# Performance work log

Measured on AMD Instinct MI355X. Metric: run time of the kernel, lower is better.

## Reference

```python
import jax, jax.numpy as jnp
import numpy as np

N_NODES = 50000
N_EDGES = 800000
D = 128


def setup_inputs() -> dict:
    key = jax.random.key(0)
    ks = jax.random.split(key, 8)
    h = jax.random.normal(ks[0], (N_NODES, D), dtype=jnp.float32)
    src = jax.random.randint(ks[1], (N_EDGES,), 0, N_NODES, dtype=jnp.int64)
    dst = jax.random.randint(ks[2], (N_EDGES,), 0, N_NODES, dtype=jnp.int64)
    # Glorot-ish init for the three GraphConv weights
    scale = 1.0 / np.sqrt(D)
    W0 = jax.random.normal(ks[3], (D, D), dtype=jnp.float32) * scale
    W1 = jax.random.normal(ks[4], (D, D), dtype=jnp.float32) * scale
    W2 = jax.random.normal(ks[5], (D, D), dtype=jnp.float32) * scale
    b0 = jnp.zeros((D,), dtype=jnp.float32)
    b1 = jnp.zeros((D,), dtype=jnp.float32)
    b2 = jnp.zeros((D,), dtype=jnp.float32)
    return {"h": h, "src": src, "dst": dst, "W0": W0, "b0": b0,
            "W1": W1, "b1": b1, "W2": W2, "b2": b2}


def _graph_conv(x, src, dst, W, b, n_nodes):
    """DGL GraphConv, norm='both', activation=ReLU.
    in_feats == out_feats -> aggregate first, then matmul W."""
    ones = jnp.ones_like(src, dtype=x.dtype)
    out_deg = jnp.clip(jax.ops.segment_sum(ones, src, num_segments=n_nodes), 1.0)
    in_deg = jnp.clip(jax.ops.segment_sum(ones, dst, num_segments=n_nodes), 1.0)
    x = x * (out_deg ** -0.5)[:, None]          # src-side normalization
    m = jax.ops.segment_sum(x[src], dst, num_segments=n_nodes)  # sparse aggregation
    m = m * (in_deg ** -0.5)[:, None]           # dst-side normalization
    return jax.nn.relu(m @ W + b)


def reference(h, src, dst, W0, b0, W1, b1, W2, b2):
    n = h.shape[0]
    h = _graph_conv(h, src, dst, W0, b0, n)
    h = _graph_conv(h, src, dst, W1, b1, n)
    h = _graph_conv(h, src, dst, W2, b2, n)
    return h
```

## Files before the change

kernel.cpp:

```cpp
#include <hip/hip_runtime.h>

#define N_NODES 50000
#define N_EDGES 800000
#define D 128
#define CAP 48
#define MS_STRIDE 132
#define QNODES 12500
#define QWORDS (QNODES / 4)
#define HISTB 1024
#define EPB (N_EDGES / 256)
#define HWORDS (N_NODES / 4)
#define FILLB ((N_EDGES + 255) / 256)
#define REDB ((HWORDS + 255) / 256)

typedef __attribute__((ext_vector_type(4))) float f32x4;
typedef __attribute__((ext_vector_type(8))) short s16x8;

__device__ inline unsigned short f32_to_bf16_rtne(float f) {
    union { float f; unsigned u; } c; c.f = f;
    unsigned u = c.u;
    u += 0x7FFF + ((u >> 16) & 1);
    return (unsigned short)(u >> 16);
}
__device__ inline float bf16_to_f32(unsigned short h) {
    union { unsigned u; float f; } c; c.u = ((unsigned)h) << 16;
    return c.f;
}
__device__ inline unsigned pack_bf2(float a, float b) {
    return (unsigned)f32_to_bf16_rtne(a) | ((unsigned)f32_to_bf16_rtne(b) << 16);
}
__device__ inline void unpack_bf2(unsigned u, float& a, float& b) {
    union { unsigned u; float f; } c0, c1;
    c0.u = u << 16; c1.u = u & 0xFFFF0000u;
    a = c0.f; b = c1.f;
}
__device__ inline void acc_uint4(uint4 v, float* a) {
    float f0, f1;
    unpack_bf2(v.x, f0, f1); a[0] += f0; a[1] += f1;
    unpack_bf2(v.y, f0, f1); a[2] += f0; a[3] += f1;
    unpack_bf2(v.z, f0, f1); a[4] += f0; a[5] += f1;
    unpack_bf2(v.w, f0, f1); a[6] += f0; a[7] += f1;
}


__global__ __launch_bounds__(256) void build_all(const int* __restrict__ src,
                                                 const int* __restrict__ dst,
                                                 int* __restrict__ cursor,
                                                 unsigned* __restrict__ partial,
                                                 int* __restrict__ slots) {
    __shared__ unsigned hist[QWORDS];
    int b = blockIdx.x;
    if (b < HISTB) {
        int q = b >> 8, p = b & 255;
        int n0 = q * QNODES;
        for (int i = threadIdx.x; i < QWORDS; i += 256) hist[i] = 0;
        __syncthreads();
        int e0 = p * EPB;
        for (int i = threadIdx.x; i < EPB; i += 256) {
            int s = src[e0 + i];
            unsigned r = (unsigned)(s - n0);
            if (r < (unsigned)QNODES) atomicAdd(&hist[r >> 2], 1u << ((r & 3) * 8));
        }
        __syncthreads();
        unsigned* dstp = partial + (size_t)b * QWORDS;
        for (int i = threadIdx.x; i < QWORDS; i += 256) dstp[i] = hist[i];
    } else {
        int e = (b - HISTB) * 256 + threadIdx.x;
        if (e < N_EDGES) {
            int d = dst[e], s = src[e];
            int pos = atomicAdd(&cursor[d], 1);
            if (pos < CAP) slots[d * CAP + pos] = s;
        }
    }
}


__global__ __launch_bounds__(256) void mid_reduce_pack(const unsigned* __restrict__ partial,
                                                       float* __restrict__ s_out,
                                                       const float* __restrict__ W0,
                                                       const float* __restrict__ W1,
                                                       const float* __restrict__ W2,
                                                       s16x8* __restrict__ wpk) {
    int blk = blockIdx.x;
    if (blk < REDB) {
        int w = blk * 256 + threadIdx.x;
        if (w >= HWORDS) return;
        int q = w / QWORDS, wq = w - q * QWORDS;
        const unsigned* base = partial + (size_t)(q * 256) * QWORDS + wq;
        int c0 = 0, c1 = 0, c2 = 0, c3 = 0;
        for (int p = 0; p < 256; p++) {
            unsigned v = base[(size_t)p * QWORDS];
            c0 += v & 255; c1 += (v >> 8) & 255; c2 += (v >> 16) & 255; c3 += v >> 24;
        }
        float4 so;
        so.x = rsqrtf(fmaxf((float)c0, 1.0f));
        so.y = rsqrtf(fmaxf((float)c1, 1.0f));
        so.z = rsqrtf(fmaxf((float)c2, 1.0f));
        so.w = rsqrtf(fmaxf((float)c3, 1.0f));
        ((float4*)s_out)[w] = so;
    } else {
        int wid = (blk - REDB) * 4 + (threadIdx.x >> 6);
        if (wid >= 96) return;
        int lane = threadIdx.x & 63;
        int layer = wid / 32, rem = wid % 32;
        int ct = rem >> 2, ks = rem & 3;
        const float* W = (layer == 0) ? W0 : (layer == 1) ? W1 : W2;
        int col = ct * 16 + (lane & 15);
        int k0  = ks * 32 + (lane >> 4) * 8;
        s16x8 hi, lo;
#pragma unroll
        for (int j = 0; j < 8; j++) {
            float w = W[(k0 + j) * D + col];
            unsigned short h = f32_to_bf16_rtne(w);
            hi[j] = (short)h;
            lo[j] = (short)f32_to_bf16_rtne(w - bf16_to_f32(h));
        }
        int idx = layer * 4096 + (ct * 4 + ks) * 64 + lane;
        wpk[idx]        = hi;
        wpk[idx + 2048] = lo;
    }
}


__global__ __launch_bounds__(256) void hconv(const float4* __restrict__ h,
                                             const float* __restrict__ s_out,
                                             uint2* __restrict__ hbA,
                                             uint2* __restrict__ hbB) {
    int gid = blockIdx.x * 256 + threadIdx.x;
    const int total = N_NODES * 32;
    if (gid < total) {
        float so = s_out[gid >> 5];
        float4 v = h[gid];
        hbA[gid] = make_uint2(pack_bf2(so * v.x, so * v.y), pack_bf2(so * v.z, so * v.w));
    } else if (gid < total + 32) {
        hbA[total + (gid - total)] = make_uint2(0u, 0u);
    } else if (gid < total + 64) {
        hbB[total + (gid - total - 32)] = make_uint2(0u, 0u);
    }
}


__global__ __launch_bounds__(256) void fused_layer(const uint4* __restrict__ x,
                                                   const int* __restrict__ slots,
                                                   const int* __restrict__ deg,
                                                   const s16x8* __restrict__ wpk,
                                                   const float* __restrict__ bias,
                                                   const float* __restrict__ s_out,
                                                   float* __restrict__ outf,
                                                   unsigned short* __restrict__ outb) {
    __shared__ float mS[16 * MS_STRIDE];
    int tid = threadIdx.x;
    int row0 = blockIdx.x * 16;

    {
        int nloc = tid >> 4;
        int l    = tid & 15;
        int node = row0 + nloc;
        int dgraw = deg[node];
        int dg = min(dgraw, CAP);
        int base = node * CAP;
        int idx0 = (l      < dg) ? slots[base + l]      : N_NODES;
        int idx1 = (16 + l < dg) ? slots[base + 16 + l] : N_NODES;
        int idx2 = (32 + l < dg) ? slots[base + 32 + l] : N_NODES;

        float a[8];
#pragma unroll
        for (int j = 0; j < 8; j++) a[j] = 0.f;

        int nr = (dg + 7) >> 3;
        for (int r = 0; r < nr; r++) {
            int c = r >> 1;
            int v = (c == 0) ? idx0 : ((c == 1) ? idx1 : idx2);
            int k = (r & 1) * 8;
            int s0 = __shfl(v, k + 0, 16), s1 = __shfl(v, k + 1, 16);
            int s2 = __shfl(v, k + 2, 16), s3 = __shfl(v, k + 3, 16);
            int s4 = __shfl(v, k + 4, 16), s5 = __shfl(v, k + 5, 16);
            int s6 = __shfl(v, k + 6, 16), s7 = __shfl(v, k + 7, 16);
            uint4 g0 = x[s0 * 16 + l];
            uint4 g1 = x[s1 * 16 + l];
            uint4 g2 = x[s2 * 16 + l];
            uint4 g3 = x[s3 * 16 + l];
            uint4 g4 = x[s4 * 16 + l];
            uint4 g5 = x[s5 * 16 + l];
            uint4 g6 = x[s6 * 16 + l];
            uint4 g7 = x[s7 * 16 + l];
            acc_uint4(g0, a); acc_uint4(g1, a); acc_uint4(g2, a); acc_uint4(g3, a);
            acc_uint4(g4, a); acc_uint4(g5, a); acc_uint4(g6, a); acc_uint4(g7, a);
        }
        float si = rsqrtf(fmaxf((float)dgraw, 1.0f));
        float* dp = &mS[nloc * MS_STRIDE + l * 8];
#pragma unroll
        for (int j = 0; j < 8; j++) dp[j] = a[j] * si;
    }
    __syncthreads();

    int wv = tid >> 6;
    int lane = tid & 63;
    int arow = lane & 15, aq = lane >> 4;
    int ct0 = wv * 2, ct1 = ct0 + 1;
    f32x4 acc0 = (f32x4)0.f, acc1 = (f32x4)0.f;

#pragma unroll
    for (int ks = 0; ks < 4; ks++) {
        const float* ap = &mS[arow * MS_STRIDE + ks * 32 + aq * 8];
        s16x8 ahi, alo;
#pragma unroll
        for (int j = 0; j < 8; j++) {
            float av = ap[j];
            unsigned short hh = f32_to_bf16_rtne(av);
            ahi[j] = (short)hh;
            alo[j] = (short)f32_to_bf16_rtne(av - bf16_to_f32(hh));
        }
        int idx0 = (ct0 * 4 + ks) * 64 + lane;
        int idx1 = (ct1 * 4 + ks) * 64 + lane;
        s16x8 b0h = wpk[idx0], b0l = wpk[idx0 + 2048];
        s16x8 b1h = wpk[idx1], b1l = wpk[idx1 + 2048];
        acc0 = __builtin_amdgcn_mfma_f32_16x16x32_bf16(ahi, b0h, acc0, 0, 0, 0);
        acc0 = __builtin_amdgcn_mfma_f32_16x16x32_bf16(alo, b0h, acc0, 0, 0, 0);
        acc0 = __builtin_amdgcn_mfma_f32_16x16x32_bf16(ahi, b0l, acc0, 0, 0, 0);
        acc1 = __builtin_amdgcn_mfma_f32_16x16x32_bf16(ahi, b1h, acc1, 0, 0, 0);
        acc1 = __builtin_amdgcn_mfma_f32_16x16x32_bf16(alo, b1h, acc1, 0, 0, 0);
        acc1 = __builtin_amdgcn_mfma_f32_16x16x32_bf16(ahi, b1l, acc1, 0, 0, 0);
    }

    int crow0 = aq * 4;
    float so4[4];
    if (outb) {
#pragma unroll
        for (int r = 0; r < 4; r++) so4[r] = s_out[row0 + crow0 + r];
    }
    int colA = ct0 * 16 + arow, colB = ct1 * 16 + arow;
    float bA = bias[colA], bB = bias[colB];
#pragma unroll
    for (int r = 0; r < 4; r++) {
        size_t rowoff = (size_t)(row0 + crow0 + r) * D;
        float vA = fmaxf(acc0[r] + bA, 0.f);
        float vB = fmaxf(acc1[r] + bB, 0.f);
        if (outf) { outf[rowoff + colA] = vA; outf[rowoff + colB] = vB; }
        if (outb) {
            outb[rowoff + colA] = f32_to_bf16_rtne(so4[r] * vA);
            outb[rowoff + colB] = f32_to_bf16_rtne(so4[r] * vB);
        }
    }
}


extern "C" void kernel_launch(void* const* d_in, const int* in_sizes, int n_in,
                              void* d_out, int out_size, void* d_ws, size_t ws_size,
                              hipStream_t stream) {
    const float* h  = (const float*)d_in[0];
    const int*  src = (const int*)d_in[1];
    const int*  dst = (const int*)d_in[2];
    const float* W0 = (const float*)d_in[3];
    const float* b0 = (const float*)d_in[4];
    const float* W1 = (const float*)d_in[5];
    const float* b1 = (const float*)d_in[6];
    const float* W2 = (const float*)d_in[7];
    const float* b2 = (const float*)d_in[8];
    float* out = (float*)d_out;

    char* w = (char*)d_ws;
    auto carve = [&](size_t bytes) -> void* {
        void* p = (void*)w;
        w += (bytes + 255) & ~(size_t)255;
        return p;
    };
    int*      cursor  = (int*)carve(N_NODES * sizeof(int));
    float*    s_out   = (float*)carve(N_NODES * sizeof(float));
    int*      slots   = (int*)carve((size_t)N_NODES * CAP * sizeof(int));
    unsigned* partial = (unsigned*)carve((size_t)HISTB * QWORDS * sizeof(unsigned));
    unsigned short* actA = (unsigned short*)carve((size_t)(N_NODES + 1) * D * 2);
    unsigned short* actB = (unsigned short*)carve((size_t)(N_NODES + 1) * D * 2);
    s16x8*    wpk     = (s16x8*)carve(3 * 4096 * sizeof(s16x8));

    hipMemsetAsync(cursor, 0, N_NODES * sizeof(int), stream);
    build_all<<<HISTB + FILLB, 256, 0, stream>>>(src, dst, cursor, partial, slots);
    mid_reduce_pack<<<REDB + 24, 256, 0, stream>>>(partial, s_out, W0, W1, W2, wpk);
    hconv<<<(N_NODES * 32 + 64 + 255) / 256, 256, 0, stream>>>((const float4*)h, s_out,
                                                               (uint2*)actA, (uint2*)actB);

    const int GRID = N_NODES / 16;

    fused_layer<<<GRID, 256, 0, stream>>>((const uint4*)actA, slots, cursor,
                                          wpk, b0, s_out, nullptr, actB);
    fused_layer<<<GRID, 256, 0, stream>>>((const uint4*)actB, slots, cursor,
                                          wpk + 4096, b1, s_out, nullptr, actA);
    fused_layer<<<GRID, 256, 0, stream>>>((const uint4*)actA, slots, cursor,
                                          wpk + 8192, b2, s_out, out, nullptr);
}
```

Baseline: 261.0 us.

## Split bf16 activations into four column-quarter planes and gather per quarter

Stores the bf16 activation tables as four separate planes, each holding a 32-column quarter for every node (64 bytes per node per plane). The aggregation loop now makes four passes, one per quarter. In each pass, 4 lanes cover a row slice and 4 edge groups run in parallel, and the partial sums are reduced with cross-lane shuffles. The aim is to shrink the gather working set per pass so it fits in cache better. The change also adds nontemporal loads and stores for slots and outputs. In exchange the slot indices are walked four times and shuffle/reduction work is added.

```diff
diff --git a/kernel.cpp b/kernel.cpp
--- a/kernel.cpp
+++ b/kernel.cpp
@@ -12,9 +12,11 @@
 #define HWORDS (N_NODES / 4)
 #define FILLB ((N_EDGES + 255) / 256)
 #define REDB ((HWORDS + 255) / 256)
+#define NP1 (N_NODES + 1)
 
 typedef __attribute__((ext_vector_type(4))) float f32x4;
 typedef __attribute__((ext_vector_type(8))) short s16x8;
+typedef __attribute__((ext_vector_type(4))) unsigned u32x4;
 
 __device__ inline unsigned short f32_to_bf16_rtne(float f) {
     union { float f; unsigned u; } c; c.f = f;
@@ -34,7 +36,7 @@
     c0.u = u << 16; c1.u = u & 0xFFFF0000u;
     a = c0.f; b = c1.f;
 }
-__device__ inline void acc_uint4(uint4 v, float* a) {
+__device__ inline void acc_u32x4(u32x4 v, float* a) {
     float f0, f1;
     unpack_bf2(v.x, f0, f1); a[0] += f0; a[1] += f1;
     unpack_bf2(v.y, f0, f1); a[2] += f0; a[3] += f1;
@@ -124,23 +126,33 @@
 
 __global__ __launch_bounds__(256) void hconv(const float4* __restrict__ h,
                                              const float* __restrict__ s_out,
-                                             uint2* __restrict__ hbA,
-                                             uint2* __restrict__ hbB) {
+                                             u32x4* __restrict__ actA,
+                                             u32x4* __restrict__ actB) {
     int gid = blockIdx.x * 256 + threadIdx.x;
-    const int total = N_NODES * 32;
+    const int total = N_NODES * 16;
     if (gid < total) {
-        float so = s_out[gid >> 5];
-        float4 v = h[gid];
-        hbA[gid] = make_uint2(pack_bf2(so * v.x, so * v.y), pack_bf2(so * v.z, so * v.w));
+        int q = gid / (N_NODES * 4);
+        int r = gid - q * (N_NODES * 4);
+        int node = r >> 2, p = r & 3;
+        int part = q * 4 + p;
+        float so = s_out[node];
+        float4 v0 = h[node * 32 + part * 2];
+        float4 v1 = h[node * 32 + part * 2 + 1];
+        u32x4 u;
+        u.x = pack_bf2(so * v0.x, so * v0.y); u.y = pack_bf2(so * v0.z, so * v0.w);
+        u.z = pack_bf2(so * v1.x, so * v1.y); u.w = pack_bf2(so * v1.z, so * v1.w);
+        __builtin_nontemporal_store(u, &actA[(size_t)(q * NP1 + node) * 4 + p]);
+    } else if (gid < total + 16) {
+        int z = gid - total;
+        actA[(size_t)((z >> 2) * NP1 + N_NODES) * 4 + (z & 3)] = (u32x4)0u;
     } else if (gid < total + 32) {
-        hbA[total + (gid - total)] = make_uint2(0u, 0u);
-    } else if (gid < total + 64) {
-        hbB[total + (gid - total - 32)] = make_uint2(0u, 0u);
-    }
-}
-
-
-__global__ __launch_bounds__(256) void fused_layer(const uint4* __restrict__ x,
+        int z = gid - total - 16;
+        actB[(size_t)((z >> 2) * NP1 + N_NODES) * 4 + (z & 3)] = (u32x4)0u;
+    }
+}
+
+
+__global__ __launch_bounds__(256) void fused_layer(const u32x4* __restrict__ x,
                                                    const int* __restrict__ slots,
                                                    const int* __restrict__ deg,
                                                    const s16x8* __restrict__ wpk,
@@ -155,42 +167,46 @@
     {
         int nloc = tid >> 4;
         int l    = tid & 15;
+        int eh   = l >> 2, p = l & 3;
         int node = row0 + nloc;
         int dgraw = deg[node];
         int dg = min(dgraw, CAP);
         int base = node * CAP;
-        int idx0 = (l      < dg) ? slots[base + l]      : N_NODES;
-        int idx1 = (16 + l < dg) ? slots[base + 16 + l] : N_NODES;
-        int idx2 = (32 + l < dg) ? slots[base + 32 + l] : N_NODES;
-
-        float a[8];
-#pragma unroll
-        for (int j = 0; j < 8; j++) a[j] = 0.f;
-
-        int nr = (dg + 7) >> 3;
-        for (int r = 0; r < nr; r++) {
-            int c = r >> 1;
-            int v = (c == 0) ? idx0 : ((c == 1) ? idx1 : idx2);
-            int k = (r & 1) * 8;
-            int s0 = __shfl(v, k + 0, 16), s1 = __shfl(v, k + 1, 16);
-            int s2 = __shfl(v, k + 2, 16), s3 = __shfl(v, k + 3, 16);
-            int s4 = __shfl(v, k + 4, 16), s5 = __shfl(v, k + 5, 16);
-            int s6 = __shfl(v, k + 6, 16), s7 = __shfl(v, k + 7, 16);
-            uint4 g0 = x[s0 * 16 + l];
-            uint4 g1 = x[s1 * 16 + l];
-            uint4 g2 = x[s2 * 16 + l];
-            uint4 g3 = x[s3 * 16 + l];
-            uint4 g4 = x[s4 * 16 + l];
-            uint4 g5 = x[s5 * 16 + l];
-            uint4 g6 = x[s6 * 16 + l];
-            uint4 g7 = x[s7 * 16 + l];
-            acc_uint4(g0, a); acc_uint4(g1, a); acc_uint4(g2, a); acc_uint4(g3, a);
-            acc_uint4(g4, a); acc_uint4(g5, a); acc_uint4(g6, a); acc_uint4(g7, a);
-        }
+        int idx0 = (l      < dg) ? __builtin_nontemporal_load(&slots[base + l])      : N_NODES;
+        int idx1 = (16 + l < dg) ? __builtin_nontemporal_load(&slots[base + 16 + l]) : N_NODES;
+        int idx2 = (32 + l < dg) ? __builtin_nontemporal_load(&slots[base + 32 + l]) : N_NODES;
         float si = rsqrtf(fmaxf((float)dgraw, 1.0f));
-        float* dp = &mS[nloc * MS_STRIDE + l * 8];
-#pragma unroll
-        for (int j = 0; j < 8; j++) dp[j] = a[j] * si;
+        int nit = (dg + 7) >> 3;
+
+        for (int q = 0; q < 4; q++) {
+            const u32x4* xq = x + (size_t)(q * NP1) * 4;
+            float a[8];
+#pragma unroll
+            for (int j = 0; j < 8; j++) a[j] = 0.f;
+            for (int it = 0; it < nit; it++) {
+                int e0 = it * 8 + eh, e1 = it * 8 + 4 + eh;
+                int c0 = e0 >> 4, k0 = e0 & 15;
+                int c1 = e1 >> 4, k1 = e1 & 15;
+                int v0 = (c0 == 0) ? idx0 : ((c0 == 1) ? idx1 : idx2);
+                int v1 = (c1 == 0) ? idx0 : ((c1 == 1) ? idx1 : idx2);
+                int s0 = __shfl(v0, k0, 16);
+                int s1 = __shfl(v1, k1, 16);
+                u32x4 g0 = xq[s0 * 4 + p];
+                u32x4 g1 = xq[s1 * 4 + p];
+                acc_u32x4(g0, a);
+                acc_u32x4(g1, a);
+            }
+#pragma unroll
+            for (int j = 0; j < 8; j++) {
+                a[j] += __shfl_xor(a[j], 4, 16);
+                a[j] += __shfl_xor(a[j], 8, 16);
+            }
+            if (eh == 0) {
+                float* dp = &mS[nloc * MS_STRIDE + q * 32 + p * 8];
+#pragma unroll
+                for (int j = 0; j < 8; j++) dp[j] = a[j] * si;
+            }
+        }
     }
     __syncthreads();
 
@@ -230,16 +246,21 @@
         for (int r = 0; r < 4; r++) so4[r] = s_out[row0 + crow0 + r];
     }
     int colA = ct0 * 16 + arow, colB = ct1 * 16 + arow;
+    int wcA = colA & 31, wcB = colB & 31;
     float bA = bias[colA], bB = bias[colB];
 #pragma unroll
     for (int r = 0; r < 4; r++) {
-        size_t rowoff = (size_t)(row0 + crow0 + r) * D;
+        int row = row0 + crow0 + r;
         float vA = fmaxf(acc0[r] + bA, 0.f);
         float vB = fmaxf(acc1[r] + bB, 0.f);
-        if (outf) { outf[rowoff + colA] = vA; outf[rowoff + colB] = vB; }
+        if (outf) {
+            __builtin_nontemporal_store(vA, &outf[(size_t)row * D + colA]);
+            __builtin_nontemporal_store(vB, &outf[(size_t)row * D + colB]);
+        }
         if (outb) {
-            outb[rowoff + colA] = f32_to_bf16_rtne(so4[r] * vA);
-            outb[rowoff + colB] = f32_to_bf16_rtne(so4[r] * vB);
+            size_t qb = (size_t)(wv * NP1 + row) * 32;
+            __builtin_nontemporal_store(f32_to_bf16_rtne(so4[r] * vA), &outb[qb + wcA]);
+            __builtin_nontemporal_store(f32_to_bf16_rtne(so4[r] * vB), &outb[qb + wcB]);
         }
     }
 }
@@ -269,22 +290,22 @@
     float*    s_out   = (float*)carve(N_NODES * sizeof(float));
     int*      slots   = (int*)carve((size_t)N_NODES * CAP * sizeof(int));
     unsigned* partial = (unsigned*)carve((size_t)HISTB * QWORDS * sizeof(unsigned));
-    unsigned short* actA = (unsigned short*)carve((size_t)(N_NODES + 1) * D * 2);
-    unsigned short* actB = (unsigned short*)carve((size_t)(N_NODES + 1) * D * 2);
+    unsigned short* actA = (unsigned short*)carve((size_t)NP1 * 256);
+    unsigned short* actB = (unsigned short*)carve((size_t)NP1 * 256);
     s16x8*    wpk     = (s16x8*)carve(3 * 4096 * sizeof(s16x8));
 
-    hipMemsetAsync(cursor, 0, N_NODES * sizeof(int), stream);
+    (void)hipMemsetAsync(cursor, 0, N_NODES * sizeof(int), stream);
     build_all<<<HISTB + FILLB, 256, 0, stream>>>(src, dst, cursor, partial, slots);
     mid_reduce_pack<<<REDB + 24, 256, 0, stream>>>(partial, s_out, W0, W1, W2, wpk);
-    hconv<<<(N_NODES * 32 + 64 + 255) / 256, 256, 0, stream>>>((const float4*)h, s_out,
-                                                               (uint2*)actA, (uint2*)actB);
+    hconv<<<(N_NODES * 16 + 32 + 255) / 256, 256, 0, stream>>>((const float4*)h, s_out,
+                                                               (u32x4*)actA, (u32x4*)actB);
 
     const int GRID = N_NODES / 16;
 
-    fused_layer<<<GRID, 256, 0, stream>>>((const uint4*)actA, slots, cursor,
+    fused_layer<<<GRID, 256, 0, stream>>>((const u32x4*)actA, slots, cursor,
                                           wpk, b0, s_out, nullptr, actB);
-    fused_layer<<<GRID, 256, 0, stream>>>((const uint4*)actB, slots, cursor,
+    fused_layer<<<GRID, 256, 0, stream>>>((const u32x4*)actB, slots, cursor,
                                           wpk + 4096, b1, s_out, nullptr, actA);
-    fused_layer<<<GRID, 256, 0, stream>>>((const uint4*)actA, slots, cursor,
+    fused_layer<<<GRID, 256, 0, stream>>>((const u32x4*)actA, slots, cursor,
                                           wpk + 8192, b2, s_out, out, nullptr);
 }
```

New measurement: 293.7 us. +12.5%, slower.

## Bucket nodes by in-degree iteration count to balance fused layer blocks

Applied to the files above, without the earlier changes.

Adds two small kernels that count nodes per gather-iteration bucket (ceil(min(deg,CAP)/8)) and scatter node ids into a permutation grouped by bucket. Each fused_layer block then processes 16 nodes of similar degree, read through the permutation, and writes outputs to the permuted rows. The aim is to cut divergence within 16-lane groups and wavefronts, where the slowest node's degree sets the loop count. The cost is two extra launches, indirect row addressing and scattered output writes.

```diff
diff --git a/kernel.cpp b/kernel.cpp
--- a/kernel.cpp
+++ b/kernel.cpp
@@ -12,6 +12,7 @@
 #define HWORDS (N_NODES / 4)
 #define FILLB ((N_EDGES + 255) / 256)
 #define REDB ((HWORDS + 255) / 256)
+#define NB 8
 
 typedef __attribute__((ext_vector_type(4))) float f32x4;
 typedef __attribute__((ext_vector_type(8))) short s16x8;
@@ -41,6 +42,7 @@
     unpack_bf2(v.z, f0, f1); a[4] += f0; a[5] += f1;
     unpack_bf2(v.w, f0, f1); a[6] += f0; a[7] += f1;
 }
+__device__ inline int nit_of(int d) { return (min(d, CAP) + 7) >> 3; }
 
 
 __global__ __launch_bounds__(256) void build_all(const int* __restrict__ src,
@@ -75,6 +77,41 @@
 }
 
 
+__global__ __launch_bounds__(256) void perm_count(const int* __restrict__ deg,
+                                                  int* __restrict__ bcnt) {
+    __shared__ int lcnt[NB];
+    if (threadIdx.x < NB) lcnt[threadIdx.x] = 0;
+    __syncthreads();
+    int i = blockIdx.x * 256 + threadIdx.x;
+    if (i < N_NODES) atomicAdd(&lcnt[nit_of(deg[i])], 1);
+    __syncthreads();
+    if (threadIdx.x < NB && lcnt[threadIdx.x]) atomicAdd(&bcnt[threadIdx.x], lcnt[threadIdx.x]);
+}
+
+__global__ __launch_bounds__(256) void perm_scatter(const int* __restrict__ deg,
+                                                    const int* __restrict__ bcnt,
+                                                    int* __restrict__ bcur,
+                                                    int* __restrict__ perm) {
+    __shared__ int lcnt[NB], resv[NB];
+    if (threadIdx.x < NB) lcnt[threadIdx.x] = 0;
+    __syncthreads();
+    int i = blockIdx.x * 256 + threadIdx.x;
+    int b = 0, lidx = 0;
+    if (i < N_NODES) {
+        b = nit_of(deg[i]);
+        lidx = atomicAdd(&lcnt[b], 1);
+    }
+    __syncthreads();
+    if (threadIdx.x < NB) {
+        int base = 0;
+        for (int j = 0; j < threadIdx.x; j++) base += bcnt[j];
+        resv[threadIdx.x] = base + (lcnt[threadIdx.x] ? atomicAdd(&bcur[threadIdx.x], lcnt[threadIdx.x]) : 0);
+    }
+    __syncthreads();
+    if (i < N_NODES) perm[resv[b] + lidx] = i;
+}
+
+
 __global__ __launch_bounds__(256) void mid_reduce_pack(const unsigned* __restrict__ partial,
                                                        float* __restrict__ s_out,
                                                        const float* __restrict__ W0,
@@ -143,19 +180,22 @@
 __global__ __launch_bounds__(256) void fused_layer(const uint4* __restrict__ x,
                                                    const int* __restrict__ slots,
                                                    const int* __restrict__ deg,
+                                                   const int* __restrict__ perm,
                                                    const s16x8* __restrict__ wpk,
                                                    const float* __restrict__ bias,
                                                    const float* __restrict__ s_out,
                                                    float* __restrict__ outf,
                                                    unsigned short* __restrict__ outb) {
     __shared__ float mS[16 * MS_STRIDE];
+    __shared__ int pS[16];
     int tid = threadIdx.x;
     int row0 = blockIdx.x * 16;
 
     {
         int nloc = tid >> 4;
         int l    = tid & 15;
-        int node = row0 + nloc;
+        int node = perm[row0 + nloc];
+        if (l == 0) pS[nloc] = node;
         int dgraw = deg[node];
         int dg = min(dgraw, CAP);
         int base = node * CAP;
@@ -224,16 +264,19 @@
     }
 
     int crow0 = aq * 4;
+    int prow[4];
     float so4[4];
+#pragma unroll
+    for (int r = 0; r < 4; r++) prow[r] = pS[crow0 + r];
     if (outb) {
 #pragma unroll
-        for (int r = 0; r < 4; r++) so4[r] = s_out[row0 + crow0 + r];
+        for (int r = 0; r < 4; r++) so4[r] = s_out[prow[r]];
     }
     int colA = ct0 * 16 + arow, colB = ct1 * 16 + arow;
     float bA = bias[colA], bB = bias[colB];
 #pragma unroll
     for (int r = 0; r < 4; r++) {
-        size_t rowoff = (size_t)(row0 + crow0 + r) * D;
+        size_t rowoff = (size_t)prow[r] * D;
         float vA = fmaxf(acc0[r] + bA, 0.f);
         float vB = fmaxf(acc1[r] + bB, 0.f);
         if (outf) { outf[rowoff + colA] = vA; outf[rowoff + colB] = vB; }
@@ -265,26 +308,32 @@
         w += (bytes + 255) & ~(size_t)255;
         return p;
     };
-    int*      cursor  = (int*)carve(N_NODES * sizeof(int));
+    int*      zr      = (int*)carve((N_NODES + 2 * NB) * sizeof(int));
+    int*      cursor  = zr;
+    int*      bcnt    = zr + N_NODES;
+    int*      bcur    = zr + N_NODES + NB;
     float*    s_out   = (float*)carve(N_NODES * sizeof(float));
+    int*      perm    = (int*)carve(N_NODES * sizeof(int));
     int*      slots   = (int*)carve((size_t)N_NODES * CAP * sizeof(int));
     unsigned* partial = (unsigned*)carve((size_t)HISTB * QWORDS * sizeof(unsigned));
     unsigned short* actA = (unsigned short*)carve((size_t)(N_NODES + 1) * D * 2);
     unsigned short* actB = (unsigned short*)carve((size_t)(N_NODES + 1) * D * 2);
     s16x8*    wpk     = (s16x8*)carve(3 * 4096 * sizeof(s16x8));
 
-    hipMemsetAsync(cursor, 0, N_NODES * sizeof(int), stream);
+    (void)hipMemsetAsync(zr, 0, (N_NODES + 2 * NB) * sizeof(int), stream);
     build_all<<<HISTB + FILLB, 256, 0, stream>>>(src, dst, cursor, partial, slots);
+    perm_count<<<(N_NODES + 255) / 256, 256, 0, stream>>>(cursor, bcnt);
+    perm_scatter<<<(N_NODES + 255) / 256, 256, 0, stream>>>(cursor, bcnt, bcur, perm);
     mid_reduce_pack<<<REDB + 24, 256, 0, stream>>>(partial, s_out, W0, W1, W2, wpk);
     hconv<<<(N_NODES * 32 + 64 + 255) / 256, 256, 0, stream>>>((const float4*)h, s_out,
                                                                (uint2*)actA, (uint2*)actB);
 
     const int GRID = N_NODES / 16;
 
-    fused_layer<<<GRID, 256, 0, stream>>>((const uint4*)actA, slots, cursor,
+    fused_layer<<<GRID, 256, 0, stream>>>((const uint4*)actA, slots, cursor, perm,
                                           wpk, b0, s_out, nullptr, actB);
-    fused_layer<<<GRID, 256, 0, stream>>>((const uint4*)actB, slots, cursor,
+    fused_layer<<<GRID, 256, 0, stream>>>((const uint4*)actB, slots, cursor, perm,
                                           wpk + 4096, b1, s_out, nullptr, actA);
-    fused_layer<<<GRID, 256, 0, stream>>>((const uint4*)actA, slots, cursor,
+    fused_layer<<<GRID, 256, 0, stream>>>((const uint4*)actA, slots, cursor, perm,
                                           wpk + 8192, b2, s_out, out, nullptr);
 }
```

Measured after the change: 272.1 us. +4.2%, slower.
